# Kernel optimization log

Hardware: AMD Instinct MI355X
Metric: run time of the kernel (lower is better)

Reference implementation:

```python
import jax, jax.numpy as jnp
import numpy as np
import math

B, T, DIM = 2, 2048, 4096
N_HEADS, N_KV_HEADS = 32, 8
HEAD_DIM = DIM // N_HEADS          # 128
N_REP = N_HEADS // N_KV_HEADS      # 4
ROPE_THETA = 500000.0
NEG_INF = -1e9


def setup_inputs() -> dict:
    key = jax.random.key(0)
    ks = jax.random.split(key, 5)
    x = jax.random.normal(ks[0], (B, T, DIM), dtype=jnp.float32)
    # rotary angles: theta_j = pos * base^(-2j/d), shape [T, HEAD_DIM//2]
    inv_freq = 1.0 / (ROPE_THETA ** (jnp.arange(0, HEAD_DIM, 2, dtype=jnp.float32) / HEAD_DIM))
    freqs = jnp.arange(T, dtype=jnp.float32)[:, None] * inv_freq[None, :]
    # causal additive mask [T, T]
    mask = jnp.where(jnp.tril(jnp.ones((T, T), dtype=bool)), 0.0, NEG_INF).astype(jnp.float32)
    s = 0.02
    wq = jax.random.normal(ks[1], (DIM, N_HEADS * HEAD_DIM), dtype=jnp.float32) * s
    wk = jax.random.normal(ks[2], (DIM, N_KV_HEADS * HEAD_DIM), dtype=jnp.float32) * s
    wv = jax.random.normal(ks[3], (DIM, N_KV_HEADS * HEAD_DIM), dtype=jnp.float32) * s
    wo = jax.random.normal(ks[4], (N_HEADS * HEAD_DIM, DIM), dtype=jnp.float32) * s
    return {"x": x, "freqs": freqs, "mask": mask, "wq": wq, "wk": wk, "wv": wv, "wo": wo, "start_pos": 0}


def _apply_rope(x, cos, sin):
    # x: [B, T, H, D]; cos/sin: [T, D//2]; adjacent pairs rotated (view-as-complex)
    xr = x[..., 0::2]
    xi = x[..., 1::2]
    c = cos[None, :, None, :]
    s = sin[None, :, None, :]
    out_r = xr * c - xi * s
    out_i = xr * s + xi * c
    return jnp.stack([out_r, out_i], axis=-1).reshape(x.shape)


def reference(x, freqs, mask, wq, wk, wv, wo, start_pos):
    Bx, Tx, C = x.shape
    xq = (x @ wq).reshape(Bx, Tx, N_HEADS, HEAD_DIM)
    xk = (x @ wk).reshape(Bx, Tx, N_KV_HEADS, HEAD_DIM)
    xv = (x @ wv).reshape(Bx, Tx, N_KV_HEADS, HEAD_DIM)
    cos, sin = jnp.cos(freqs), jnp.sin(freqs)
    xq = _apply_rope(xq, cos, sin)
    xk = _apply_rope(xk, cos, sin)
    # repeat_kv for GQA: [B, T, Hkv, D] -> [B, T, Hkv*n_rep, D]
    xk = jnp.repeat(xk, N_REP, axis=2)
    xv = jnp.repeat(xv, N_REP, axis=2)
    q = xq.transpose(0, 2, 1, 3)  # [B, H, T, D]
    k = xk.transpose(0, 2, 1, 3)
    v = xv.transpose(0, 2, 1, 3)
    scores = jnp.einsum("bhtd,bhsd->bhts", q, k) / math.sqrt(HEAD_DIM)
    scores = scores + mask[None, None, :, :]
    probs = jax.nn.softmax(scores.astype(jnp.float32), axis=-1).astype(q.dtype)
    out = jnp.einsum("bhts,bhsd->bhtd", probs, v)
    out = out.transpose(0, 2, 1, 3).reshape(Bx, Tx, -1)
    return out @ wo
```

## Files before the change

### kernel.cpp

```cpp
#include <hip/hip_runtime.h>
#include <cstdint>
#include <cstddef>

typedef float  f32x4  __attribute__((ext_vector_type(4)));
typedef short  bf16x8 __attribute__((ext_vector_type(8)));
typedef unsigned short u16;
typedef u16    u16x8  __attribute__((ext_vector_type(8)));
typedef unsigned int u32;

#define T_SEQ 2048
#define N_HEADS 32
#define N_KVH 8
#define HD 128

__device__ __forceinline__ u16 f2bf(float f){
  union { float f; unsigned u; } v; v.f = f;
  unsigned u = v.u;
  u += 0x7fffu + ((u >> 16) & 1u);
  return (u16)(u >> 16);
}

__device__ __forceinline__ u32 cvt_pk_bf16(float a, float b){
  u32 r;
  asm volatile("v_cvt_pk_bf16_f32 %0, %1, %2" : "=v"(r) : "v"(a), "v"(b));
  return r;
}

__device__ __forceinline__ void gll16(const void* g, void* l){
  __builtin_amdgcn_global_load_lds((const __attribute__((address_space(1))) void*)g,
                                   (__attribute__((address_space(3))) void*)l, 16, 0, 0);
}

__global__ void mk_tables(const float* __restrict__ f, float* __restrict__ c, float* __restrict__ s){
  int i = blockIdx.x*256 + threadIdx.x;
  float v = f[i];
  c[i] = cosf(v);
  s[i] = sinf(v);
}

__global__ void cvt_bf16(const float* __restrict__ in, u16* __restrict__ out){
  size_t i = (size_t)blockIdx.x*256 + threadIdx.x;
  const float4* p = (const float4*)(in + i*8);
  float4 a = p[0], b = p[1];
  u16x8 o;
  o[0]=f2bf(a.x); o[1]=f2bf(a.y); o[2]=f2bf(a.z); o[3]=f2bf(a.w);
  o[4]=f2bf(b.x); o[5]=f2bf(b.y); o[6]=f2bf(b.z); o[7]=f2bf(b.w);
  *(u16x8*)(out + i*8) = o;
}

__global__ void wtrans(const float* __restrict__ W, u16* __restrict__ Wt, int K, int N){
  __shared__ float t[32][33];
  int tx = threadIdx.x, ty = threadIdx.y;
  int nb = blockIdx.x*32, kb = blockIdx.y*32;
#pragma unroll
  for (int j=0;j<4;j++) t[ty+8*j][tx] = W[(size_t)(kb+ty+8*j)*N + nb + tx];
  __syncthreads();
#pragma unroll
  for (int j=0;j<4;j++) Wt[(size_t)(nb+ty+8*j)*K + kb + tx] = f2bf(t[tx][ty+8*j]);
}

template<int BN>
__global__ __launch_bounds__(512, 2) void gemm256(
    const u16* __restrict__ A, const u16* __restrict__ Bt,
    float* __restrict__ C, int N, int K)
{
  constexpr int NGB = BN/64;
  constexpr int NF  = BN/64;
  __shared__ u16 Ab[2][16384];
  __shared__ u16 Bb[2][BN*64];
  const int tid = threadIdx.x;
  const int w = tid >> 6, lane = tid & 63;
  const int lo = lane & 15, hi = lane >> 4;

  const int nbx = N / BN;
  const int cpx = (int)gridDim.x >> 3;
  const int swzb = ((int)blockIdx.x & 7)*cpx + ((int)blockIdx.x >> 3);
  const int bx = swzb % nbx, by = swzb / nbx;
  const int m0 = by << 8, n0 = bx * BN;
  const int wm = w >> 2, wn = w & 3;

  const int rA = tid >> 3;
  const int chg = (tid & 7) ^ (rA & 7);
  const size_t srcoff = (size_t)rA * K + chg*8;
  const u16* Ag = A  + (size_t)m0*K + srcoff;
  const u16* Bg = Bt + (size_t)n0*K + srcoff;
  const int dstc = (w*64)*8;

  f32x4 acc[8][NF];
#pragma unroll
  for (int i=0;i<8;i++)
#pragma unroll
    for (int j=0;j<NF;j++) acc[i][j] = (f32x4){0.f,0.f,0.f,0.f};

  const int NT = K >> 6;
#pragma unroll
  for (int j=0;j<4;j++)   gll16(Ag + (size_t)j*64*K, &Ab[0][j*4096 + dstc]);
#pragma unroll
  for (int j=0;j<NGB;j++) gll16(Bg + (size_t)j*64*K, &Bb[0][j*4096 + dstc]);

  const int sw = lo & 7;
#pragma unroll 1
  for (int t=0; t<NT; ++t){
    const int cur = t & 1;
    if (t > 0){
      asm volatile("s_waitcnt lgkmcnt(0)" ::: "memory");
      __builtin_amdgcn_s_barrier();
    }
    if (t + 1 < NT){
      const int kt = (t+1) << 6;
      const int nxt = cur ^ 1;
#pragma unroll
      for (int j=0;j<4;j++)   gll16(Ag + (size_t)j*64*K + kt, &Ab[nxt][j*4096 + dstc]);
#pragma unroll
      for (int j=0;j<NGB;j++) gll16(Bg + (size_t)j*64*K + kt, &Bb[nxt][j*4096 + dstc]);
      if constexpr (BN == 256){
        asm volatile("s_waitcnt vmcnt(8)" ::: "memory");
      } else {
        asm volatile("s_waitcnt vmcnt(6)" ::: "memory");
      }
    } else {
      asm volatile("s_waitcnt vmcnt(0)" ::: "memory");
    }
    __builtin_amdgcn_s_barrier();
    __builtin_amdgcn_sched_barrier(0);

    const u16* Ac = &Ab[cur][0] + (wm*128)*64;
    const u16* Bc = &Bb[cur][0] + (wn*(BN/4))*64;
    bf16x8 a[4], b[NF];
#pragma unroll
    for (int ks=0; ks<2; ks++){
      const int ch = ((ks*4 + hi) ^ sw) << 3;
#pragma unroll
      for (int g=0; g<NF; g++) b[g] = *(const bf16x8*)(Bc + (g*16 + lo)*64 + ch);
#pragma unroll
      for (int mh=0; mh<2; mh++){
#pragma unroll
        for (int f=0; f<4; f++) a[f] = *(const bf16x8*)(Ac + (mh*64 + f*16 + lo)*64 + ch);
        __builtin_amdgcn_s_setprio(1);
#pragma unroll
        for (int f=0; f<4; f++)
#pragma unroll
          for (int g=0; g<NF; g++)
            acc[mh*4+f][g] = __builtin_amdgcn_mfma_f32_16x16x32_bf16(a[f], b[g], acc[mh*4+f][g], 0, 0, 0);
        __builtin_amdgcn_s_setprio(0);
      }
    }
  }

#pragma unroll
  for (int mh=0; mh<2; mh++)
#pragma unroll
    for (int f=0; f<4; f++)
#pragma unroll
      for (int g=0; g<NF; g++)
#pragma unroll
        for (int r=0; r<4; r++)
          C[(size_t)(m0 + wm*128 + mh*64 + f*16 + hi*4 + r)*N + n0 + wn*(BN/4) + g*16 + lo] = acc[mh*4+f][g][r];
}

#define DSA8(MH, RG) { _Pragma("unroll") for (int f=0; f<4; f++) a[f] = *(const bf16x8*)(AL + (RG) + La[MH][f]); }
#define DSB8(RG)     { _Pragma("unroll") for (int g=0; g<4; g++) b[g] = *(const bf16x8*)(BL + (RG) + Lb[g]); }
#define STGA8(RG, KO) { gll16(Ag + offs0 + (KO), AL + (RG) + wofs); gll16(Ag + offs1 + (KO), AL + (RG) + 4096 + wofs); }
#define STGB8(RG, KO) { gll16(Bg + offs0 + (KO), BL + (RG) + wofs); gll16(Bg + offs1 + (KO), BL + (RG) + 4096 + wofs); }
#define MFMA16(MH) { _Pragma("unroll") for (int f=0; f<4; f++) _Pragma("unroll") for (int g=0; g<4; g++) \
    acc[(MH)*4+f][g] = __builtin_amdgcn_mfma_f32_16x16x32_bf16(a[f], b[g], acc[(MH)*4+f][g], 0, 0, 0); }
#define PH_SYNC() { __builtin_amdgcn_sched_barrier(0); __builtin_amdgcn_s_barrier(); \
    asm volatile("s_waitcnt lgkmcnt(0)" ::: "memory"); __builtin_amdgcn_sched_barrier(0); }
#define PH_END() { __builtin_amdgcn_s_setprio(0); __builtin_amdgcn_s_barrier(); }

__global__ __launch_bounds__(512, 2) void gemm8p(
    const u16* __restrict__ A, const u16* __restrict__ Bt,
    float* __restrict__ C, int N, int K)
{
  __shared__ u16 AL[32768];
  __shared__ u16 BL[32768];
  const int tid = threadIdx.x;
  const int w = tid >> 6, lane = tid & 63;
  const int lo = lane & 15, hi = lane >> 4;

  const int nbx = N >> 8;
  const int cpx = (int)gridDim.x >> 3;
  const int swzb = ((int)blockIdx.x & 7)*cpx + ((int)blockIdx.x >> 3);
  const int bx = swzb % nbx, by = swzb / nbx;
  const int m0 = by << 8, n0 = bx << 8;
  const int wm = w >> 2, wn = w & 3;

  int La[2][4], Lb[4];
#pragma unroll
  for (int mh=0; mh<2; mh++)
#pragma unroll
    for (int f=0; f<4; f++){
      int row = wm*128 + mh*64 + f*16 + lo;
      int p = row >> 1;
      La[mh][f] = (p*8 + (((row&1)*4 + hi) ^ (p&7)))*8;
    }
#pragma unroll
  for (int g=0; g<4; g++){
    int row = wn*64 + g*16 + lo;
    int p = row >> 1;
    Lb[g] = (p*8 + (((row&1)*4 + hi) ^ (p&7)))*8;
  }

  int offs0, offs1;
  {
    int n = tid;
    int p = n>>3, e = (n&7) ^ (p&7);
    offs0 = (p*2 + (e>>2))*K + (e&3)*8;
    n = 512 + tid;
    p = n>>3; e = (n&7) ^ (p&7);
    offs1 = (p*2 + (e>>2))*K + (e&3)*8;
  }
  const u16* Ag = A  + (size_t)m0*K;
  const u16* Bg = Bt + (size_t)n0*K;
  const int wofs = w*512;

  f32x4 acc[8][4];
#pragma unroll
  for (int i=0;i<8;i++)
#pragma unroll
    for (int j=0;j<4;j++) acc[i][j] = (f32x4){0.f,0.f,0.f,0.f};

  const int NT = K >> 6;
  bf16x8 a[4], b[4];

  STGA8(0, 0)       STGB8(0, 0)
  STGA8(8192, 32)   STGB8(8192, 32)
  STGA8(16384, 64)  STGB8(16384, 64)
  asm volatile("s_waitcnt vmcnt(8)" ::: "memory");
  __builtin_amdgcn_s_barrier();

#pragma unroll 1
  for (int u = 0; u < NT-2; u += 2){
    const int ku = u*64;
    DSA8(0, 0) DSB8(0)
    STGA8(24576, ku+96)
    PH_SYNC() __builtin_amdgcn_s_setprio(1); MFMA16(0) PH_END()
    DSA8(1, 0)
    STGB8(24576, ku+96)
    asm volatile("s_waitcnt vmcnt(8)" ::: "memory");
    PH_SYNC() __builtin_amdgcn_s_setprio(1); MFMA16(1) PH_END()
    DSA8(0, 8192) DSB8(8192)
    STGA8(0, ku+128)
    PH_SYNC() __builtin_amdgcn_s_setprio(1); MFMA16(0) PH_END()
    DSA8(1, 8192)
    STGB8(0, ku+128)
    asm volatile("s_waitcnt vmcnt(8)" ::: "memory");
    PH_SYNC() __builtin_amdgcn_s_setprio(1); MFMA16(1) PH_END()
    DSA8(0, 16384) DSB8(16384)
    STGA8(8192, ku+160)
    PH_SYNC() __builtin_amdgcn_s_setprio(1); MFMA16(0) PH_END()
    DSA8(1, 16384)
    STGB8(8192, ku+160)
    asm volatile("s_waitcnt vmcnt(8)" ::: "memory");
    PH_SYNC() __builtin_amdgcn_s_setprio(1); MFMA16(1) PH_END()
    DSA8(0, 24576) DSB8(24576)
    STGA8(16384, ku+192)
    PH_SYNC() __builtin_amdgcn_s_setprio(1); MFMA16(0) PH_END()
    DSA8(1, 24576)
    STGB8(16384, ku+192)
    asm volatile("s_waitcnt vmcnt(8)" ::: "memory");
    PH_SYNC() __builtin_amdgcn_s_setprio(1); MFMA16(1) PH_END()
  }

  {
    const int ku = (NT-2)*64;
    DSA8(0, 0) DSB8(0)
    STGA8(24576, ku+96)
    PH_SYNC() __builtin_amdgcn_s_setprio(1); MFMA16(0) PH_END()
    DSA8(1, 0)
    STGB8(24576, ku+96)
    asm volatile("s_waitcnt vmcnt(8)" ::: "memory");
    PH_SYNC() __builtin_amdgcn_s_setprio(1); MFMA16(1) PH_END()
    DSA8(0, 8192) DSB8(8192)
    PH_SYNC() __builtin_amdgcn_s_setprio(1); MFMA16(0) PH_END()
    DSA8(1, 8192)
    asm volatile("s_waitcnt vmcnt(4)" ::: "memory");
    PH_SYNC() __builtin_amdgcn_s_setprio(1); MFMA16(1) PH_END()
    DSA8(0, 16384) DSB8(16384)
    PH_SYNC() __builtin_amdgcn_s_setprio(1); MFMA16(0) PH_END()
    DSA8(1, 16384)
    asm volatile("s_waitcnt vmcnt(0)" ::: "memory");
    PH_SYNC() __builtin_amdgcn_s_setprio(1); MFMA16(1) PH_END()
    DSA8(0, 24576) DSB8(24576)
    PH_SYNC() __builtin_amdgcn_s_setprio(1); MFMA16(0) PH_END()
    DSA8(1, 24576)
    PH_SYNC() __builtin_amdgcn_s_setprio(1); MFMA16(1) PH_END()
  }

#pragma unroll
  for (int mh=0; mh<2; mh++)
#pragma unroll
    for (int f=0; f<4; f++)
#pragma unroll
      for (int g=0; g<4; g++)
#pragma unroll
        for (int r=0; r<4; r++)
          C[(size_t)(m0 + wm*128 + mh*64 + f*16 + hi*4 + r)*N + n0 + wn*64 + g*16 + lo] = acc[mh*4+f][g][r];
}

__global__ void rope_q(const float* __restrict__ qf, const float* __restrict__ c,
                       const float* __restrict__ s, u16* __restrict__ qb){
  const int row = blockIdx.x;
  const int t = row & (T_SEQ-1);
  const float* ib = qf + (size_t)row*4096;
  u16* ob = qb + (size_t)row*4096;
#pragma unroll
  for (int k=0;k<8;k++){
    int p = threadIdx.x + k*256;
    int i = p & 63;
    float cv = c[t*64+i], sv = s[t*64+i];
    float2 v = *(const float2*)(ib + 2*p);
    float vr = v.x*cv - v.y*sv;
    float vi = v.x*sv + v.y*cv;
    ushort2 o; o.x = f2bf(vr*0.12751743648963412f); o.y = f2bf(vi*0.12751743648963412f);
    *(ushort2*)(ob + 2*p) = o;
  }
}

__global__ void rope_k(const float* __restrict__ kvf, const float* __restrict__ c,
                       const float* __restrict__ s, u16* __restrict__ kb){
  const int row = blockIdx.x;
  const int b = row >> 11, t = row & (T_SEQ-1);
  const float* ib = kvf + (size_t)row*2048;
#pragma unroll
  for (int k=0;k<2;k++){
    int p = threadIdx.x + k*256;
    int kvh = p >> 6, i = p & 63;
    float cv = c[t*64+i], sv = s[t*64+i];
    float2 v = *(const float2*)(ib + 2*p);
    float vr = v.x*cv - v.y*sv;
    float vi = v.x*sv + v.y*cv;
    u16* o = kb + ((size_t)(b*N_KVH+kvh)*T_SEQ + t)*HD + 2*i;
    ushort2 ov; ov.x = f2bf(vr); ov.y = f2bf(vi);
    *(ushort2*)o = ov;
  }
}

__global__ void vtrans(const float* __restrict__ kvf, u16* __restrict__ vt){
  __shared__ float tl[32][33];
  int tx = threadIdx.x, ty = threadIdx.y;
  int t0 = blockIdx.x*32, d0 = blockIdx.y*32, bh = blockIdx.z;
  int b = bh >> 3, kvh = bh & 7;
#pragma unroll
  for (int j=0;j<4;j++)
    tl[ty+8*j][tx] = kvf[(size_t)(b*T_SEQ + t0+ty+8*j)*2048 + 1024 + kvh*HD + d0 + tx];
  __syncthreads();
#pragma unroll
  for (int j=0;j<4;j++)
    vt[((size_t)bh*HD + d0+ty+8*j)*T_SEQ + t0 + tx] = f2bf(tl[tx][ty+8*j]);
}

#define KVB 64
__global__ __launch_bounds__(512) void attn_kernel(
    const u16* __restrict__ qb, const u16* __restrict__ kb,
    const u16* __restrict__ vt, u16* __restrict__ attn)
{
  __shared__ u16 KV[2][2][8192];

  const int tid = threadIdx.x;
  const int lane = tid & 63, wid = tid >> 6;
  const int lo = lane & 15, hi = lane >> 4;
  const bool lowhi = (hi < 2);
  const int bp0 = lo + 32*(hi & 1);
  const int bp1 = bp0 + 16;
  const int h = blockIdx.y, b = blockIdx.z;
  const int kvh = h >> 2;
  const int qt = b ? (int)blockIdx.x : 7 - (int)blockIdx.x;
  const int q0 = qt*256 + wid*32;
  const int ntiles = (qt+1)*4;

  int koff[2], voff[2];
#pragma unroll
  for (int p=0;p<2;p++){
    int s = p*512 + tid;
    int kr = s >> 4, kch = (s & 15) ^ (kr & 7);
    koff[p] = kr*HD + kch*8;
    int vd = s >> 3, vch = (s & 7) ^ (vd & 7);
    voff[p] = vd*T_SEQ + vch*8;
  }
  const u16* Kg = kb + (size_t)(b*N_KVH + kvh)*T_SEQ*HD;
  const u16* Vg = vt + (size_t)(b*N_KVH + kvh)*HD*T_SEQ;

  bf16x8 qfr[2][4];
#pragma unroll
  for (int mb=0;mb<2;mb++){
    const u16* qrow = qb + (size_t)(b*T_SEQ + q0 + mb*16 + lo)*4096 + h*HD;
#pragma unroll
    for (int kc=0;kc<4;kc++) qfr[mb][kc] = *(const bf16x8*)(qrow + kc*32 + hi*8);
  }

  f32x4 acc[2][8];
#pragma unroll
  for (int mb=0;mb<2;mb++)
#pragma unroll
    for (int nd=0;nd<8;nd++) acc[mb][nd] = (f32x4){0.f,0.f,0.f,0.f};
  float m_[2] = {-3.0e38f, -3.0e38f};
  float l_[2] = {0.f, 0.f};

#pragma unroll
  for (int p=0;p<2;p++){
    gll16(Kg + koff[p], (u16*)&KV[0][0][0] + (p*512 + wid*64)*8);
    gll16(Vg + voff[p], (u16*)&KV[0][1][0] + (p*512 + wid*64)*8);
  }

#pragma unroll 1
  for (int st=0; st<ntiles; ++st){
    const int cur = st & 1;
    const int sb = st*KVB;
    if (st > 0){
      asm volatile("s_waitcnt lgkmcnt(0)" ::: "memory");
      __builtin_amdgcn_s_barrier();
    }
    if (st + 1 < ntiles){
      const int nxt = cur ^ 1;
      const int nb2 = (st+1)*KVB;
#pragma unroll
      for (int p=0;p<2;p++){
        gll16(Kg + nb2*HD + koff[p], (u16*)&KV[nxt][0][0] + (p*512 + wid*64)*8);
        gll16(Vg + nb2    + voff[p], (u16*)&KV[nxt][1][0] + (p*512 + wid*64)*8);
      }
      asm volatile("s_waitcnt vmcnt(4)" ::: "memory");
    } else {
      asm volatile("s_waitcnt vmcnt(0)" ::: "memory");
    }
    __builtin_amdgcn_s_barrier();

    const bool live = (sb <= q0 + 31);
    if (live){
      f32x4 sc[2][4];
#pragma unroll
      for (int mb=0;mb<2;mb++)
#pragma unroll
        for (int ns=0;ns<4;ns++) sc[mb][ns] = (f32x4){0.f,0.f,0.f,0.f};
      __builtin_amdgcn_s_setprio(1);
#pragma unroll
      for (int ns=0;ns<4;ns++){
        const int row = ns*16 + lo;
        const u16* klp = (const u16*)&KV[cur][0][0] + row*HD;
        const int sw = row & 7;
        bf16x8 kf[4];
#pragma unroll
        for (int kc=0;kc<4;kc++) kf[kc] = *(const bf16x8*)(klp + (((kc*4+hi)^sw)<<3));
#pragma unroll
        for (int kc=0;kc<4;kc++){
          sc[0][ns] = __builtin_amdgcn_mfma_f32_16x16x32_bf16(kf[kc], qfr[0][kc], sc[0][ns], 0, 0, 0);
          sc[1][ns] = __builtin_amdgcn_mfma_f32_16x16x32_bf16(kf[kc], qfr[1][kc], sc[1][ns], 0, 0, 0);
        }
      }
      __builtin_amdgcn_s_setprio(0);

      if (sb + 63 > q0){
#pragma unroll
        for (int mb=0;mb<2;mb++){
          const int qg = q0 + mb*16 + lo;
#pragma unroll
          for (int ns=0;ns<4;ns++)
#pragma unroll
            for (int r=0;r<4;r++){
              int sg = sb + ns*16 + hi*4 + r;
              if (sg > qg) sc[mb][ns][r] = -3.0e38f;
            }
        }
      }

      bf16x8 pa[2][2];
#pragma unroll
      for (int mb=0;mb<2;mb++){
        float mx = fmaxf(fmaxf(fmaxf(sc[mb][0][0],sc[mb][0][1]),fmaxf(sc[mb][0][2],sc[mb][0][3])),
                   fmaxf(fmaxf(fmaxf(sc[mb][1][0],sc[mb][1][1]),fmaxf(sc[mb][1][2],sc[mb][1][3])),
                         fmaxf(fmaxf(sc[mb][2][0],sc[mb][2][1]),
                               fmaxf(fmaxf(sc[mb][2][2],sc[mb][2][3]),
                                     fmaxf(fmaxf(sc[mb][3][0],sc[mb][3][1]),fmaxf(sc[mb][3][2],sc[mb][3][3]))))));
        mx = fmaxf(mx, __shfl_xor(mx, 16));
        mx = fmaxf(mx, __shfl_xor(mx, 32));
        if (__any(mx > m_[mb] + 8.f)){
          float mn = fmaxf(m_[mb], mx);
          float scal = exp2f(m_[mb] - mn);
          m_[mb] = mn;
          l_[mb] *= scal;
          float srow[4];
#pragma unroll
          for (int r=0;r<4;r++) srow[r] = __shfl(scal, hi*4+r);
#pragma unroll
          for (int nd=0;nd<8;nd++)
#pragma unroll
            for (int r=0;r<4;r++) acc[mb][nd][r] *= srow[r];
        }
        float rs = 0.f;
#pragma unroll
        for (int ns=0;ns<4;ns++)
#pragma unroll
          for (int r=0;r<4;r++){
            sc[mb][ns][r] = exp2f(sc[mb][ns][r] - m_[mb]);
            rs += sc[mb][ns][r];
          }
        rs += __shfl_xor(rs, 16);
        rs += __shfl_xor(rs, 32);
        l_[mb] += rs;

#pragma unroll
        for (int k2=0;k2<2;k2++){
          u32 P0 = cvt_pk_bf16(sc[mb][2*k2][0],   sc[mb][2*k2][1]);
          u32 P1 = cvt_pk_bf16(sc[mb][2*k2][2],   sc[mb][2*k2][3]);
          u32 Q0 = cvt_pk_bf16(sc[mb][2*k2+1][0], sc[mb][2*k2+1][1]);
          u32 Q1 = cvt_pk_bf16(sc[mb][2*k2+1][2], sc[mb][2*k2+1][3]);
          u32 pA0 = (u32)__shfl((int)P0, bp0);
          u32 pA1 = (u32)__shfl((int)P1, bp0);
          u32 pA2 = (u32)__shfl((int)P0, bp1);
          u32 pA3 = (u32)__shfl((int)P1, bp1);
          u32 qA0 = (u32)__shfl((int)Q0, bp0);
          u32 qA1 = (u32)__shfl((int)Q1, bp0);
          u32 qA2 = (u32)__shfl((int)Q0, bp1);
          u32 qA3 = (u32)__shfl((int)Q1, bp1);
          union { u32 w[4]; bf16x8 v; } pk;
          pk.w[0] = lowhi ? pA0 : qA0;
          pk.w[1] = lowhi ? pA1 : qA1;
          pk.w[2] = lowhi ? pA2 : qA2;
          pk.w[3] = lowhi ? pA3 : qA3;
          pa[mb][k2] = pk.v;
        }
      }

      __builtin_amdgcn_s_setprio(1);
#pragma unroll
      for (int nd=0;nd<8;nd++){
        const int d = nd*16 + lo;
        const u16* vlp = (const u16*)&KV[cur][1][0] + d*64;
        const int sw = d & 7;
        bf16x8 vf[2];
#pragma unroll
        for (int k2=0;k2<2;k2++) vf[k2] = *(const bf16x8*)(vlp + (((k2*4+hi)^sw)<<3));
#pragma unroll
        for (int k2=0;k2<2;k2++){
          acc[0][nd] = __builtin_amdgcn_mfma_f32_16x16x32_bf16(pa[0][k2], vf[k2], acc[0][nd], 0, 0, 0);
          acc[1][nd] = __builtin_amdgcn_mfma_f32_16x16x32_bf16(pa[1][k2], vf[k2], acc[1][nd], 0, 0, 0);
        }
      }
      __builtin_amdgcn_s_setprio(0);
    }
  }

#pragma unroll
  for (int mb=0;mb<2;mb++){
    float inv = 1.f / l_[mb];
    float invr[4];
#pragma unroll
    for (int r=0;r<4;r++) invr[r] = __shfl(inv, hi*4+r);
    u16* ob = attn + (size_t)(b*T_SEQ + q0 + mb*16 + hi*4)*4096 + h*HD;
#pragma unroll
    for (int nd=0;nd<8;nd++)
#pragma unroll
      for (int r=0;r<4;r++)
        ob[(size_t)r*4096 + nd*16 + lo] = f2bf(acc[mb][nd][r]*invr[r]);
  }
}

extern "C" void kernel_launch(void* const* d_in, const int* in_sizes, int n_in,
                              void* d_out, int out_size, void* d_ws, size_t ws_size,
                              hipStream_t stream)
{
  (void)in_sizes; (void)n_in; (void)out_size; (void)ws_size;
  const float* x     = (const float*)d_in[0];
  const float* freqs = (const float*)d_in[1];
  const float* wq    = (const float*)d_in[3];
  const float* wk    = (const float*)d_in[4];
  const float* wv    = (const float*)d_in[5];
  const float* wo    = (const float*)d_in[6];

  char* ws = (char*)d_ws;
  float* cost = (float*)(ws + 0);
  float* sint = (float*)(ws + 524288);
  u16* xb   = (u16*)(ws + 1048576);
  u16* wqt  = (u16*)(ws + 34603008);
  u16* wkt  = (u16*)(ws + 68157440);
  u16* wvt  = (u16*)(ws + 76546048);
  u16* qbuf = (u16*)(ws + 84934656);
  u16* kbuf = (u16*)(ws + 118489088);
  u16* vbuf = (u16*)(ws + 126877696);
  u16* attnb = xb;
  u16* wot   = wqt;

  float* qf  = (float*)d_out;
  float* kvf = (float*)d_out;

  dim3 tb(32, 8);

  mk_tables<<<512, 256, 0, stream>>>(freqs, cost, sint);
  cvt_bf16<<<8192, 256, 0, stream>>>(x, xb);
  wtrans<<<dim3(128,128), tb, 0, stream>>>(wq, wqt, 4096, 4096);
  wtrans<<<dim3(32,128),  tb, 0, stream>>>(wk, wkt, 4096, 1024);
  wtrans<<<dim3(32,128),  tb, 0, stream>>>(wv, wvt, 4096, 1024);

  gemm8p<<<dim3(256), 512, 0, stream>>>(xb, wqt, qf, 4096, 4096);
  rope_q<<<4096, 256, 0, stream>>>(qf, cost, sint, qbuf);

  gemm256<128><<<dim3(256), 512, 0, stream>>>(xb, wkt, kvf, 2048, 4096);
  rope_k<<<4096, 256, 0, stream>>>(kvf, cost, sint, kbuf);
  vtrans<<<dim3(64,4,16), tb, 0, stream>>>(kvf, vbuf);

  attn_kernel<<<dim3(8,32,2), 512, 0, stream>>>(qbuf, kbuf, vbuf, attnb);

  wtrans<<<dim3(128,128), tb, 0, stream>>>(wo, wot, 4096, 4096);
  gemm8p<<<dim3(256), 512, 0, stream>>>(attnb, wot, (float*)d_out, 4096, 4096);
}
```

Before: 564.8 us.

## Use transposed 16x16x16 MFMA for PV to drop P shuffles, transpose output via LDS

The PV product is recomputed as a transposed 16x16x16 bf16 MFMA, with V as the A operand and P as the B operand. P values then stay in the registers that computed them, which removes the per-tile cross-lane shuffles that repacked P into the 16x16x32 operand layout and the per-row rescale shuffles. Because the accumulator is now transposed, the epilogue stages each 16-column slice through LDS and writes out rows. The trade is twice as many MFMA instructions at half the K each, smaller V LDS reads, and added LDS traffic and barriers in the epilogue.

```diff
diff --git a/kernel.cpp b/kernel.cpp
--- a/kernel.cpp
+++ b/kernel.cpp
@@ -4,6 +4,7 @@
 
 typedef float  f32x4  __attribute__((ext_vector_type(4)));
 typedef short  bf16x8 __attribute__((ext_vector_type(8)));
+typedef short  bf16x4 __attribute__((ext_vector_type(4)));
 typedef unsigned short u16;
 typedef u16    u16x8  __attribute__((ext_vector_type(8)));
 typedef unsigned int u32;
@@ -24,6 +25,15 @@
   u32 r;
   asm volatile("v_cvt_pk_bf16_f32 %0, %1, %2" : "=v"(r) : "v"(a), "v"(b));
   return r;
+}
+
+__device__ __forceinline__ f32x4 mfma16x16x16(bf16x4 a, bf16x4 b, f32x4 c){
+#if __has_builtin(__builtin_amdgcn_mfma_f32_16x16x16bf16_1k)
+  return __builtin_amdgcn_mfma_f32_16x16x16bf16_1k(a, b, c, 0, 0, 0);
+#else
+  asm volatile("v_mfma_f32_16x16x16_bf16 %0, %1, %2, %0" : "+v"(c) : "v"(a), "v"(b));
+  return c;
+#endif
 }
 
 __device__ __forceinline__ void gll16(const void* g, void* l){
@@ -360,9 +370,6 @@
   const int tid = threadIdx.x;
   const int lane = tid & 63, wid = tid >> 6;
   const int lo = lane & 15, hi = lane >> 4;
-  const bool lowhi = (hi < 2);
-  const int bp0 = lo + 32*(hi & 1);
-  const int bp1 = bp0 + 16;
   const int h = blockIdx.y, b = blockIdx.z;
   const int kvh = h >> 2;
   const int qt = b ? (int)blockIdx.x : 7 - (int)blockIdx.x;
@@ -463,7 +470,7 @@
         }
       }
 
-      bf16x8 pa[2][2];
+      bf16x4 pb[2][4];
 #pragma unroll
       for (int mb=0;mb<2;mb++){
         float mx = fmaxf(fmaxf(fmaxf(sc[mb][0][0],sc[mb][0][1]),fmaxf(sc[mb][0][2],sc[mb][0][3])),
@@ -478,13 +485,10 @@
           float scal = exp2f(m_[mb] - mn);
           m_[mb] = mn;
           l_[mb] *= scal;
-          float srow[4];
-#pragma unroll
-          for (int r=0;r<4;r++) srow[r] = __shfl(scal, hi*4+r);
 #pragma unroll
           for (int nd=0;nd<8;nd++)
 #pragma unroll
-            for (int r=0;r<4;r++) acc[mb][nd][r] *= srow[r];
+            for (int r=0;r<4;r++) acc[mb][nd][r] *= scal;
         }
         float rs = 0.f;
 #pragma unroll
@@ -499,25 +503,11 @@
         l_[mb] += rs;
 
 #pragma unroll
-        for (int k2=0;k2<2;k2++){
-          u32 P0 = cvt_pk_bf16(sc[mb][2*k2][0],   sc[mb][2*k2][1]);
-          u32 P1 = cvt_pk_bf16(sc[mb][2*k2][2],   sc[mb][2*k2][3]);
-          u32 Q0 = cvt_pk_bf16(sc[mb][2*k2+1][0], sc[mb][2*k2+1][1]);
-          u32 Q1 = cvt_pk_bf16(sc[mb][2*k2+1][2], sc[mb][2*k2+1][3]);
-          u32 pA0 = (u32)__shfl((int)P0, bp0);
-          u32 pA1 = (u32)__shfl((int)P1, bp0);
-          u32 pA2 = (u32)__shfl((int)P0, bp1);
-          u32 pA3 = (u32)__shfl((int)P1, bp1);
-          u32 qA0 = (u32)__shfl((int)Q0, bp0);
-          u32 qA1 = (u32)__shfl((int)Q1, bp0);
-          u32 qA2 = (u32)__shfl((int)Q0, bp1);
-          u32 qA3 = (u32)__shfl((int)Q1, bp1);
-          union { u32 w[4]; bf16x8 v; } pk;
-          pk.w[0] = lowhi ? pA0 : qA0;
-          pk.w[1] = lowhi ? pA1 : qA1;
-          pk.w[2] = lowhi ? pA2 : qA2;
-          pk.w[3] = lowhi ? pA3 : qA3;
-          pa[mb][k2] = pk.v;
+        for (int ns=0;ns<4;ns++){
+          union { u32 w[2]; bf16x4 v; } pk;
+          pk.w[0] = cvt_pk_bf16(sc[mb][ns][0], sc[mb][ns][1]);
+          pk.w[1] = cvt_pk_bf16(sc[mb][ns][2], sc[mb][ns][3]);
+          pb[mb][ns] = pk.v;
         }
       }
 
@@ -525,33 +515,44 @@
 #pragma unroll
       for (int nd=0;nd<8;nd++){
         const int d = nd*16 + lo;
-        const u16* vlp = (const u16*)&KV[cur][1][0] + d*64;
         const int sw = d & 7;
-        bf16x8 vf[2];
-#pragma unroll
-        for (int k2=0;k2<2;k2++) vf[k2] = *(const bf16x8*)(vlp + (((k2*4+hi)^sw)<<3));
-#pragma unroll
-        for (int k2=0;k2<2;k2++){
-          acc[0][nd] = __builtin_amdgcn_mfma_f32_16x16x32_bf16(pa[0][k2], vf[k2], acc[0][nd], 0, 0, 0);
-          acc[1][nd] = __builtin_amdgcn_mfma_f32_16x16x32_bf16(pa[1][k2], vf[k2], acc[1][nd], 0, 0, 0);
+        const u16* vlp = (const u16*)&KV[cur][1][0] + d*64 + (hi&1)*4;
+        bf16x4 va[4];
+#pragma unroll
+        for (int ns=0;ns<4;ns++)
+          va[ns] = *(const bf16x4*)(vlp + ((((ns<<1)+(hi>>1)) ^ sw)<<3));
+#pragma unroll
+        for (int ns=0;ns<4;ns++){
+          acc[0][nd] = mfma16x16x16(va[ns], pb[0][ns], acc[0][nd]);
+          acc[1][nd] = mfma16x16x16(va[ns], pb[1][ns], acc[1][nd]);
         }
       }
       __builtin_amdgcn_s_setprio(0);
     }
   }
 
-#pragma unroll
-  for (int mb=0;mb<2;mb++){
-    float inv = 1.f / l_[mb];
-    float invr[4];
-#pragma unroll
-    for (int r=0;r<4;r++) invr[r] = __shfl(inv, hi*4+r);
-    u16* ob = attn + (size_t)(b*T_SEQ + q0 + mb*16 + hi*4)*4096 + h*HD;
-#pragma unroll
-    for (int nd=0;nd<8;nd++)
+  asm volatile("s_waitcnt lgkmcnt(0)" ::: "memory");
+  __builtin_amdgcn_s_barrier();
+  float* tb = (float*)&KV[0][0][0] + wid*544;
+  float inv[2] = {1.f/l_[0], 1.f/l_[1]};
+#pragma unroll 1
+  for (int nd=0; nd<8; nd++){
+#pragma unroll
+    for (int mb=0;mb<2;mb++)
 #pragma unroll
       for (int r=0;r<4;r++)
-        ob[(size_t)r*4096 + nd*16 + lo] = f2bf(acc[mb][nd][r]*invr[r]);
+        tb[(mb*16 + lo)*17 + hi*4 + r] = acc[mb][nd][r]*inv[mb];
+    asm volatile("s_waitcnt lgkmcnt(0)" ::: "memory");
+    __builtin_amdgcn_sched_barrier(0);
+#pragma unroll
+    for (int mb=0;mb<2;mb++){
+      u16* ob = attn + (size_t)(b*T_SEQ + q0 + mb*16 + hi*4)*4096 + h*HD + nd*16;
+#pragma unroll
+      for (int r=0;r<4;r++)
+        ob[(size_t)r*4096 + lo] = f2bf(tb[(mb*16 + hi*4 + r)*17 + lo]);
+    }
+    asm volatile("s_waitcnt lgkmcnt(0)" ::: "memory");
+    __builtin_amdgcn_sched_barrier(0);
   }
 }
 
```

Measured after the change: 588.8 us. 4.3% more time.
